# Kernel optimization log

Measured on AMD Instinct MI355X. Metric: run time of the kernel, lower is better.

The kernel has to match this reference:

```python
import jax, jax.numpy as jnp
import numpy as np

NUM_DISKS = 5
BUFFER_DIST = 0.2
DECAY_RATE = 0.9


def setup_inputs() -> dict:
    key = jax.random.key(0)
    kY, kL, kW = jax.random.split(key, 3)
    B, N, T, D = 4, 64, 80, 6
    Y = jax.random.normal(kY, (B, N, T, D), dtype=jnp.float32)
    # spread agent positions over ~tens of meters so some pairs collide, most don't
    Y = Y.at[..., :2].multiply(20.0)
    # realistic vehicle extents (meters)
    length = 3.0 + 2.0 * jax.random.uniform(kL, (B, N), dtype=jnp.float32)
    width = 1.5 + 1.0 * jax.random.uniform(kW, (B, N), dtype=jnp.float32)
    return {"Y": Y, "length": length, "width": width}


def _collision_loss(Y, length, width):
    B, N, T, _ = Y.shape
    K = NUM_DISKS
    pos = Y[..., :2]            # [B,N,T,2]
    yaw = Y[..., 4]             # [B,N,T]

    # per-agent disk layout along the body x-axis
    agt_rad = width / 2.0                                   # [B,N]
    cent_min = -(length / 2.0) + agt_rad                    # [B,N]
    cent_max = (length / 2.0) - agt_rad                     # [B,N]
    frac = jnp.arange(K, dtype=Y.dtype) / (K - 1)           # [K]
    cent_x = cent_min[..., None] + (cent_max - cent_min)[..., None] * frac  # [B,N,K]

    # rotate local [x,0] by row-vector @ [[c,-s],[s,c]] -> (x*c, -x*s), then translate
    c = jnp.cos(yaw)            # [B,N,T]
    s = jnp.sin(yaw)
    wx = cent_x[:, :, None, :] * c[:, :, :, None] + pos[..., 0][..., None]   # [B,N,T,K]
    wy = -cent_x[:, :, None, :] * s[:, :, :, None] + pos[..., 1][..., None]  # [B,N,T,K]
    w = jnp.stack([wx, wy], axis=-1)                        # [B,N,T,K,2]

    # block-diagonal pairwise distances: only same-timestep disk pairs
    sq = jnp.sum(w * w, axis=-1)                            # [B,N,T,K]
    cross = jnp.einsum('bitkc,bjtlc->bijtkl', w, w)         # [B,N,N,T,K,K]
    d2 = sq[:, :, None, :, :, None] + sq[:, None, :, :, None, :] - 2.0 * cross
    d2 = jnp.maximum(d2, 0.0)
    pos_mask = d2 > 1e-12
    dist = jnp.where(pos_mask, jnp.sqrt(jnp.where(pos_mask, d2, 1.0)), 0.0)
    pair_dists = jnp.min(dist, axis=(-2, -1))               # [B,N,N,T]

    penalty_dists = agt_rad[:, :, None] + agt_rad[:, None, :] + BUFFER_DIST  # [B,N,N]
    off_diag = ~jnp.eye(N, dtype=bool)[None, :, :, None]    # [1,N,N,1]
    is_colliding = (pair_dists <= penalty_dists[..., None]) & off_diag
    penalties = 1.0 - pair_dists / penalty_dists[..., None]
    penalties = jnp.where(is_colliding, jax.nn.relu(penalties), 0.0)

    agent_penalties = jnp.sum(penalties, axis=2)            # [B,N,T]
    exp_w = DECAY_RATE ** jnp.arange(T, dtype=Y.dtype)
    exp_w = exp_w / jnp.sum(exp_w)
    return jnp.mean(agent_penalties * exp_w[None, None, :])


def reference(Y, length, width):
    return _collision_loss(Y, length, width)
```

## Files before the change

kernel.cpp:

```cpp
#include <hip/hip_runtime.h>
#include <math.h>

#define BB 4
#define NN 64
#define TT 80
#define DD 6
#define KK 5
#define BUFFER_DIST 0.2f
#define CHUNKS 4
#define NPART (BB * TT * CHUNKS)
#define MAGIC 0x5AC0FFEEu
#define LOG2_DECAY (-0.15200309f)

typedef float v2f __attribute__((ext_vector_type(2)));

__global__ __launch_bounds__(256) void collision_kernel(
    const float* __restrict__ Y,
    const float* __restrict__ length,
    const float* __restrict__ width,
    unsigned long long* __restrict__ slots,
    float* __restrict__ out,
    float scale)
{
    const int blk   = blockIdx.x;
    const int bt    = blk >> 2;
    const int chunk = blk & 3;
    const int b = bt / TT;
    const int t = bt - b * TT;
    const int tid = threadIdx.x;

    __shared__ float2 w[KK][NN];
    __shared__ float rad[NN];

    {
        const int n  = tid & 63;
        const int kk = tid >> 6;
        const float* y = Y + (((size_t)(b * NN + n) * TT + t) * DD);
        const float2 pxy = *reinterpret_cast<const float2*>(y);
        const float yaw = y[4];
        const float c = cosf(yaw);
        const float s = sinf(yaw);
        const float L = length[b * NN + n];
        const float W = width[b * NN + n];
        const float ar = 0.5f * W;
        if (kk == 0) rad[n] = ar;
        const float cmin = -(0.5f * L) + ar;
        const float span = (0.5f * L - ar) - cmin;
        {
            const float frac = (float)kk / (float)(KK - 1);
            const float cx = cmin + span * frac;
            w[kk][n] = make_float2(fmaf(cx, c, pxy.x), fmaf(-cx, s, pxy.y));
        }
        if (kk == 0) {
            const float cx = cmin + span * 1.0f;
            w[4][n] = make_float2(fmaf(cx, c, pxy.x), fmaf(-cx, s, pxy.y));
        }
    }
    __syncthreads();

    float sum = 0.0f;
    #pragma unroll
    for (int iter = 0; iter < 2; ++iter) {
        const int p = chunk * 512 + iter * 256 + tid;
        const int r = p >> 6;
        const int c = p & 63;
        const int mask = (c <= r) ? 63 : 0;
        const int i = r ^ mask;
        const int j = c ^ mask;

        float2 wi[KK];
        #pragma unroll
        for (int k = 0; k < KK; ++k) wi[k] = w[k][i];
        const v2f wix01 = { wi[0].x, wi[1].x };
        const v2f wix23 = { wi[2].x, wi[3].x };
        const v2f wiy01 = { wi[0].y, wi[1].y };
        const v2f wiy23 = { wi[2].y, wi[3].y };
        const float wix4 = wi[4].x, wiy4 = wi[4].y;

        float m0 = 3.4e38f, m1 = 3.4e38f, m2 = 3.4e38f, m3 = 3.4e38f, m4 = 3.4e38f;
        #pragma unroll
        for (int l = 0; l < KK; ++l) {
            const float2 wj = w[l][j];
            const v2f wjx = { wj.x, wj.x };
            const v2f wjy = { wj.y, wj.y };
            const v2f dx01 = wix01 - wjx, dy01 = wiy01 - wjy;
            const v2f dx23 = wix23 - wjx, dy23 = wiy23 - wjy;
            const v2f d01 = dx01 * dx01 + dy01 * dy01;
            const v2f d23 = dx23 * dx23 + dy23 * dy23;
            m0 = fminf(m0, d01.x); m1 = fminf(m1, d01.y);
            m2 = fminf(m2, d23.x); m3 = fminf(m3, d23.y);
            const float dx4 = wix4 - wj.x, dy4 = wiy4 - wj.y;
            m4 = fminf(m4, fmaf(dx4, dx4, dy4 * dy4));
        }
        const float mind2 = fminf(fminf(fminf(m0, m1), fminf(m2, m3)), m4);

        const float pd = rad[i] + rad[j] + BUFFER_DIST;
        if (mind2 <= pd * pd && i != j) {
            const float dist = (mind2 > 1e-12f) ? sqrtf(mind2) : 0.0f;
            sum += 1.0f - dist / pd;
        }
    }

    #pragma unroll
    for (int off = 32; off > 0; off >>= 1)
        sum += __shfl_down(sum, off, 64);
    __shared__ float wsum[4];
    const int wave = tid >> 6;
    const int lane = tid & 63;
    if (lane == 0) wsum[wave] = sum;
    __syncthreads();
    if (tid == 0) {
        const float tot = wsum[0] + wsum[1] + wsum[2] + wsum[3];
        const unsigned long long payload =
            ((unsigned long long)MAGIC << 32) | (unsigned long long)__float_as_uint(tot);
        __hip_atomic_store(&slots[blk], payload, __ATOMIC_RELAXED, __HIP_MEMORY_SCOPE_AGENT);
    }

    if (blk == 0) {
        __syncthreads();
        float s = 0.0f;
        #pragma unroll
        for (int it = 0; it < NPART / 256; ++it) {
            const int idx = it * 256 + tid;
            unsigned long long v =
                __hip_atomic_load(&slots[idx], __ATOMIC_RELAXED, __HIP_MEMORY_SCOPE_AGENT);
            while ((unsigned)(v >> 32) != MAGIC) {
                __builtin_amdgcn_s_sleep(8);
                v = __hip_atomic_load(&slots[idx], __ATOMIC_RELAXED, __HIP_MEMORY_SCOPE_AGENT);
            }
            const float pv = __uint_as_float((unsigned)(v & 0xFFFFFFFFull));
            const int t2 = (idx >> 2) % TT;
            s = fmaf(pv, exp2f((float)t2 * LOG2_DECAY), s);
        }
        #pragma unroll
        for (int off = 32; off > 0; off >>= 1)
            s += __shfl_down(s, off, 64);
        __shared__ float rsum[4];
        if (lane == 0) rsum[wave] = s;
        __syncthreads();
        if (tid == 0)
            out[0] = (rsum[0] + rsum[1] + rsum[2] + rsum[3]) * scale;
    }
}

extern "C" void kernel_launch(void* const* d_in, const int* in_sizes, int n_in,
                              void* d_out, int out_size, void* d_ws, size_t ws_size,
                              hipStream_t stream) {
    const float* Y      = (const float*)d_in[0];
    const float* length = (const float*)d_in[1];
    const float* width  = (const float*)d_in[2];
    float* out = (float*)d_out;
    unsigned long long* slots = (unsigned long long*)d_ws;

    const double denom = (1.0 - pow(0.9, 80.0)) / (1.0 - 0.9);
    const float scale = (float)(2.0 / ((double)(BB * NN * TT) * denom));

    collision_kernel<<<NPART, 256, 0, stream>>>(Y, length, width, slots, out, scale);
}
```

Before: 10.54 us.

## Replace 5x5 disk distance search with nearest-disk projection per j disk

Instead of evaluating all 25 disk-pair distances, each j disk is projected onto agent i's body axis, and the nearest i disk index is found by rounding and clamping. Only that disk's distance is computed, giving 5 distances per pair instead of 25. Per-agent pose and disk-layout parameters are stored in shared memory as float4 so the projection can be done. The exchange is extra transcendental-free arithmetic (rint, clamp), a reciprocal of span that is infinite when span is zero, and possible ties that round differently from the exhaustive min.

```diff
diff --git a/kernel.cpp b/kernel.cpp
--- a/kernel.cpp
+++ b/kernel.cpp
@@ -30,7 +30,9 @@
     const int tid = threadIdx.x;
 
     __shared__ float2 w[KK][NN];
-    __shared__ float rad[NN];
+    __shared__ float4 par0[NN];
+    __shared__ float4 par1[NN];
+    __shared__ float  rad[NN];
 
     {
         const int n  = tid & 63;
@@ -38,22 +40,25 @@
         const float* y = Y + (((size_t)(b * NN + n) * TT + t) * DD);
         const float2 pxy = *reinterpret_cast<const float2*>(y);
         const float yaw = y[4];
-        const float c = cosf(yaw);
-        const float s = sinf(yaw);
+        const float cth = cosf(yaw);
+        const float sth = sinf(yaw);
         const float L = length[b * NN + n];
         const float W = width[b * NN + n];
         const float ar = 0.5f * W;
-        if (kk == 0) rad[n] = ar;
         const float cmin = -(0.5f * L) + ar;
         const float span = (0.5f * L - ar) - cmin;
         {
-            const float frac = (float)kk / (float)(KK - 1);
+            const float frac = (float)kk * 0.25f;
             const float cx = cmin + span * frac;
-            w[kk][n] = make_float2(fmaf(cx, c, pxy.x), fmaf(-cx, s, pxy.y));
+            w[kk][n] = make_float2(fmaf(cx, cth, pxy.x), fmaf(-cx, sth, pxy.y));
         }
         if (kk == 0) {
             const float cx = cmin + span * 1.0f;
-            w[4][n] = make_float2(fmaf(cx, c, pxy.x), fmaf(-cx, s, pxy.y));
+            w[4][n] = make_float2(fmaf(cx, cth, pxy.x), fmaf(-cx, sth, pxy.y));
+            const float sp = span * 0.25f;
+            par0[n] = make_float4(pxy.x, pxy.y, cth, sth);
+            par1[n] = make_float4(cmin, sp, 1.0f / sp, ar);
+            rad[n] = ar;
         }
     }
     __syncthreads();
@@ -62,39 +67,58 @@
     #pragma unroll
     for (int iter = 0; iter < 2; ++iter) {
         const int p = chunk * 512 + iter * 256 + tid;
-        const int r = p >> 6;
-        const int c = p & 63;
-        const int mask = (c <= r) ? 63 : 0;
+        const int r  = p >> 6;
+        const int cc = p & 63;
+        const int mask = (cc <= r) ? 63 : 0;
         const int i = r ^ mask;
-        const int j = c ^ mask;
+        const int j = cc ^ mask;
 
-        float2 wi[KK];
+        const float4 P0 = par0[i];
+        const float4 P1 = par1[i];
+        const float e = -P1.x * P1.z;
+        const float radj = rad[j];
+
+        float2 wj[KK];
         #pragma unroll
-        for (int k = 0; k < KK; ++k) wi[k] = w[k][i];
-        const v2f wix01 = { wi[0].x, wi[1].x };
-        const v2f wix23 = { wi[2].x, wi[3].x };
-        const v2f wiy01 = { wi[0].y, wi[1].y };
-        const v2f wiy23 = { wi[2].y, wi[3].y };
-        const float wix4 = wi[4].x, wiy4 = wi[4].y;
+        for (int l = 0; l < KK; ++l) wj[l] = w[l][j];
 
-        float m0 = 3.4e38f, m1 = 3.4e38f, m2 = 3.4e38f, m3 = 3.4e38f, m4 = 3.4e38f;
-        #pragma unroll
-        for (int l = 0; l < KK; ++l) {
-            const float2 wj = w[l][j];
-            const v2f wjx = { wj.x, wj.x };
-            const v2f wjy = { wj.y, wj.y };
-            const v2f dx01 = wix01 - wjx, dy01 = wiy01 - wjy;
-            const v2f dx23 = wix23 - wjx, dy23 = wiy23 - wjy;
-            const v2f d01 = dx01 * dx01 + dy01 * dy01;
-            const v2f d23 = dx23 * dx23 + dy23 * dy23;
-            m0 = fminf(m0, d01.x); m1 = fminf(m1, d01.y);
-            m2 = fminf(m2, d23.x); m3 = fminf(m3, d23.y);
-            const float dx4 = wix4 - wj.x, dy4 = wiy4 - wj.y;
-            m4 = fminf(m4, fmaf(dx4, dx4, dy4 * dy4));
-        }
-        const float mind2 = fminf(fminf(fminf(m0, m1), fminf(m2, m3)), m4);
+        const v2f px2 = { P0.x, P0.x }, py2 = { P0.y, P0.y };
+        const v2f c2  = { P0.z, P0.z }, s2  = { P0.w, P0.w };
 
-        const float pd = rad[i] + rad[j] + BUFFER_DIST;
+        const v2f vx01 = v2f{ wj[0].x, wj[1].x } - px2;
+        const v2f vy01 = v2f{ wj[0].y, wj[1].y } - py2;
+        const v2f vx23 = v2f{ wj[2].x, wj[3].x } - px2;
+        const v2f vy23 = v2f{ wj[2].y, wj[3].y } - py2;
+        const v2f t01 = vx01 * c2 - vy01 * s2;
+        const v2f t23 = vx23 * c2 - vy23 * s2;
+        const v2f isp2 = { P1.z, P1.z }, e2 = { e, e };
+        const v2f u01 = t01 * isp2 + e2;
+        const v2f u23 = t23 * isp2 + e2;
+        const v2f k01 = { fminf(fmaxf(rintf(u01.x), 0.0f), 4.0f),
+                          fminf(fmaxf(rintf(u01.y), 0.0f), 4.0f) };
+        const v2f k23 = { fminf(fmaxf(rintf(u23.x), 0.0f), 4.0f),
+                          fminf(fmaxf(rintf(u23.y), 0.0f), 4.0f) };
+        const v2f sp2 = { P1.y, P1.y }, cm2 = { P1.x, P1.x };
+        const v2f a01 = k01 * sp2 + cm2;
+        const v2f a23 = k23 * sp2 + cm2;
+        const v2f dx01 = vx01 - a01 * c2;
+        const v2f dy01 = vy01 + a01 * s2;
+        const v2f dx23 = vx23 - a23 * c2;
+        const v2f dy23 = vy23 + a23 * s2;
+        const v2f d01 = dx01 * dx01 + dy01 * dy01;
+        const v2f d23 = dx23 * dx23 + dy23 * dy23;
+        const float vx4 = wj[4].x - P0.x, vy4 = wj[4].y - P0.y;
+        const float t4 = vx4 * P0.z - vy4 * P0.w;
+        const float u4 = fmaf(t4, P1.z, e);
+        const float k4 = fminf(fmaxf(rintf(u4), 0.0f), 4.0f);
+        const float a4 = fmaf(k4, P1.y, P1.x);
+        const float dx4 = fmaf(-a4, P0.z, vx4);
+        const float dy4 = fmaf(a4, P0.w, vy4);
+        const float d4 = fmaf(dx4, dx4, dy4 * dy4);
+
+        const float mind2 = fminf(fminf(fminf(d01.x, d01.y), fminf(d23.x, d23.y)), d4);
+
+        const float pd = P1.w + radj + BUFFER_DIST;
         if (mind2 <= pd * pd && i != j) {
             const float dist = (mind2 > 1e-12f) ? sqrtf(mind2) : 0.0f;
             sum += 1.0f - dist / pd;
```

Result: faster. 10.15 us, median of 2 (-3.7%).
